# Performance work log

Measured on AMD Instinct MI355X. Metric: run time of the kernel, lower is better.

Reference implementation:

```python
import jax, jax.numpy as jnp
import numpy as np

N_NODES = 50000
N_EDGES = 800000
IN_FEATS = 128
OUT_FEATS = 128
FREQ_DIM = OUT_FEATS // 2 + 1
BN_EPS = 1e-5


def setup_inputs() -> dict:
    key = jax.random.key(0)
    ks = jax.random.split(key, 8)
    x = jax.random.normal(ks[0], (N_NODES, IN_FEATS), dtype=jnp.float32)
    edge_index = jax.random.randint(ks[1], (2, N_EDGES), 0, N_NODES, dtype=jnp.int64)
    # lin_fusion: Linear(2*in_feats, out_feats)
    W_fuse = jax.random.normal(ks[2], (OUT_FEATS, 2 * IN_FEATS), dtype=jnp.float32) * (1.0 / np.sqrt(2 * IN_FEATS))
    b_fuse = jnp.zeros((OUT_FEATS,), dtype=jnp.float32)
    # lin_in: Linear(in_feats, out_feats)
    W_in = jax.random.normal(ks[3], (OUT_FEATS, IN_FEATS), dtype=jnp.float32) * (1.0 / np.sqrt(IN_FEATS))
    b_in = jnp.zeros((OUT_FEATS,), dtype=jnp.float32)
    complex_weight = jax.random.normal(ks[4], (FREQ_DIM, 2), dtype=jnp.float32) * 0.02
    alpha = jnp.float32(0.5)
    gamma = jnp.ones((OUT_FEATS,), dtype=jnp.float32)
    beta = jnp.zeros((OUT_FEATS,), dtype=jnp.float32)
    return {"x": x, "edge_index": edge_index, "W_fuse": W_fuse, "b_fuse": b_fuse,
            "W_in": W_in, "b_in": b_in, "complex_weight": complex_weight,
            "alpha": alpha, "gamma": gamma, "beta": beta}


def reference(x, edge_index, W_fuse, b_fuse, W_in, b_in, complex_weight, alpha, gamma, beta):
    N = x.shape[0]
    src, dst = edge_index[0], edge_index[1]
    # --- spatial branch: scatter-mean aggregation of neighbor features ---
    msgs = x[src]  # [E, in] gather
    agg_sum = jax.ops.segment_sum(msgs, dst, num_segments=N)  # [N, in]
    cnt = jax.ops.segment_sum(jnp.ones((src.shape[0],), dtype=x.dtype), dst, num_segments=N)
    aggs = agg_sum / jnp.maximum(cnt, 1.0)[:, None]
    combined = jnp.concatenate([x, aggs], axis=1)  # [N, 2*in]
    x_spatial = combined @ W_fuse.T + b_fuse  # [N, out]
    # --- spectral branch: linear -> rfft * complex weight -> irfft ---
    h = x @ W_in.T + b_in  # [N, out]
    hf = jnp.fft.rfft(h, axis=-1)  # [N, out//2+1]
    w = complex_weight[:, 0] + 1j * complex_weight[:, 1]
    x_spectral = jnp.fft.irfft(hf * w, n=h.shape[-1], axis=-1).astype(x.dtype)
    # --- fuse + BatchNorm1d (training stats, biased var) + exact GELU ---
    out = x_spatial + alpha * x_spectral
    mean = jnp.mean(out, axis=0)
    var = jnp.mean(jnp.square(out - mean), axis=0)
    out = (out - mean) / jnp.sqrt(var + BN_EPS) * gamma + beta
    return jax.nn.gelu(out, approximate=False)
```

## Files before the change

kernel.cpp:

```cpp
#include <hip/hip_runtime.h>
#include <hip/hip_bf16.h>

#define NN 50000
#define NE 800000
#define FD 128
#define FREQ 65
#define CAP 64
#define BN_EPS 1e-5f

#define NB_PACK 3125
#define NB_CVT  6250
#define NB_WCB  128
#define NGRP 8
#define GRPN 6250
#define NCHUNK 256
#define CHUNKE 3125

typedef unsigned int u32;
typedef unsigned short u16;
typedef __attribute__((ext_vector_type(8))) short short8;
typedef __attribute__((ext_vector_type(4))) float float4v;
typedef __attribute__((ext_vector_type(2))) float floatx2;

__device__ __forceinline__ float bf2f(u16 v) {
    return __uint_as_float(((u32)v) << 16);
}
__device__ __forceinline__ u16 f2bf(float f) {
    u32 u = __float_as_uint(f);
    u32 lsb = (u >> 16) & 1u;
    return (u16)((u + 0x7fffu + lsb) >> 16);
}
__device__ __forceinline__ float ldf(const void* p, int i, int f32) {
    return f32 ? ((const float*)p)[i] : bf2f(((const u16*)p)[i]);
}
__device__ __forceinline__ int detect_f32(const void* gamma) {
    return ((const u32*)gamma)[0] == 0x3F800000u;
}
__device__ __forceinline__ int detect_idx64(const int* idx) {
    return (idx[1] | idx[3] | idx[5] | idx[7] |
            idx[9] | idx[11] | idx[13] | idx[15]) == 0;
}

__device__ __forceinline__ u32 pk4_e4m3(float a, float b, float c, float d) {
#if __has_builtin(__builtin_amdgcn_cvt_pk_fp8_f32)
    int r = __builtin_amdgcn_cvt_pk_fp8_f32(a, b, 0, false);
    r = __builtin_amdgcn_cvt_pk_fp8_f32(c, d, r, true);
    return (u32)r;
#else
    auto one = [](float f) -> u32 {
        u32 u = __float_as_uint(f);
        u32 s = (u >> 24) & 0x80u;
        float af = fabsf(f);
        if (af > 448.f) return s | 0x7Eu;
        if (af < 7.8125e-3f) return s;
        int e = (int)((u >> 23) & 255) - 127;
        u32 m = (u >> 20) & 7u;
        u32 rnd = (u >> 19) & 1u;
        u32 sticky = (u & 0x7FFFFu) ? 1u : 0u;
        m += (rnd & (sticky | (m & 1u)));
        u32 ee = (u32)(e + 7);
        if (m > 7u) { m = 0u; ee += 1u; }
        if (ee > 15u) return s | 0x7Eu;
        return s | (ee << 3) | m;
    };
    return one(a) | (one(b) << 8) | (one(c) << 16) | (one(d) << 24);
#endif
}
__device__ __forceinline__ void deq4_e4m3(u32 p, float& a, float& b, float& c, float& d) {
#if __has_builtin(__builtin_amdgcn_cvt_pk_f32_fp8)
    floatx2 lo = __builtin_amdgcn_cvt_pk_f32_fp8((int)p, false);
    floatx2 hi = __builtin_amdgcn_cvt_pk_f32_fp8((int)p, true);
    a = lo.x; b = lo.y; c = hi.x; d = hi.y;
#else
    auto one = [](u32 v) -> float {
        u32 s = (v & 0x80u) << 24;
        u32 e = (v >> 3) & 15u;
        u32 m = v & 7u;
        if (e == 0) {
            float f = (float)m * 0.001953125f;
            return s ? -f : f;
        }
        return __uint_as_float(s | ((e + 120u) << 23) | (m << 20));
    };
    a = one(p & 255u); b = one((p >> 8) & 255u);
    c = one((p >> 16) & 255u); d = one(p >> 24);
#endif
}

#define WS_WCB       0
#define WS_BIAS      65536
#define WS_ZSTART    66048
#define WS_BNSUM     66048
#define WS_BNSQ      66560
#define WS_DEG       67072
#define WS_ZEND      267072
#define WS_CSR16     267136
#define WS_EPACK     6667136
#define WS_X8        9867136
#define WS_OUT16     16267136

__global__ __launch_bounds__(256) void prep_kernel(const void* __restrict__ x,
                                                   const int* __restrict__ idx,
                                                   const void* __restrict__ Wf,
                                                   const void* __restrict__ bfu,
                                                   const void* __restrict__ Wi,
                                                   const void* __restrict__ bi,
                                                   const void* __restrict__ cw,
                                                   const void* __restrict__ alpha_p,
                                                   const void* __restrict__ gamma,
                                                   u32* __restrict__ epack,
                                                   u32* __restrict__ x8,
                                                   u16* __restrict__ WcB,
                                                   float* __restrict__ bias) {
    int b = blockIdx.x;
    int t = threadIdx.x;
    if (b < NB_PACK) {
        int e = b * 256 + t;
        int src, dst;
        if (detect_idx64(idx)) { src = idx[2 * e]; dst = idx[2 * NE + 2 * e]; }
        else                   { src = idx[e];     dst = idx[NE + e]; }
        epack[e] = ((u32)dst << 16) | (u32)src;
        return;
    }
    b -= NB_PACK;
    if (b < NB_CVT) {
        int gid = b * 256 + t;
        float a, bb, c, d;
        if (detect_f32(gamma)) {
            float4 v = ((const float4*)x)[gid];
            a = v.x; bb = v.y; c = v.z; d = v.w;
        } else {
            uint2 v = ((const uint2*)x)[gid];
            a = bf2f((u16)(v.x & 0xffffu)); bb = bf2f((u16)(v.x >> 16));
            c = bf2f((u16)(v.y & 0xffffu)); d = bf2f((u16)(v.y >> 16));
        }
        x8[gid] = pk4_e4m3(a, bb, c, d);
        return;
    }
    b -= NB_CVT;
    int f32 = detect_f32(gamma);
    int j = b;
    __shared__ float wr[FREQ], wi[FREQ];
    __shared__ float cl[128];
    __shared__ float part[256];
    if (t < FREQ) { wr[t] = ldf(cw, 2 * t, f32); wi[t] = ldf(cw, 2 * t + 1, f32); }
    __syncthreads();
    if (t < 128) {
        float s = wr[0] + ((t & 1) ? -wr[64] : wr[64]);
        for (int f = 1; f < 64; ++f) {
            int ph = (f * t) & 127;
            float th = (float)ph * (6.283185307179586f / 128.f);
            float sn, cs;
            sincosf(th, &sn, &cs);
            s += 2.f * (wr[f] * cs - wi[f] * sn);
        }
        cl[t] = s * (1.f / 128.f);
    }
    __syncthreads();
    int k = t & 127, mh = t >> 7;
    float acc = 0.f;
    int m0 = mh * 64;
#pragma unroll 8
    for (int mm = 0; mm < 64; ++mm) {
        int m = m0 + mm;
        acc = fmaf(ldf(Wi, m * 128 + k, f32), cl[(j - m) & 127], acc);
    }
    part[t] = acc;
    __syncthreads();
    if (t < 128) {
        float al = ldf(alpha_p, 0, f32);
        int ct = j >> 4;
        float v = ldf(Wf, j * 256 + k, f32) + al * (part[k] + part[k + 128]);
        int off = (((ct * 8 + (k >> 5)) * 64) + ((k >> 3) & 3) * 16 + (j & 15)) * 8 + (k & 7);
        WcB[off] = f2bf(v);
        int k2 = k + 128;
        float v2 = ldf(Wf, j * 256 + k2, f32);
        int off2 = (((ct * 8 + (k2 >> 5)) * 64) + ((k2 >> 3) & 3) * 16 + (j & 15)) * 8 + (k2 & 7);
        WcB[off2] = f2bf(v2);
        if (j == 0) {
            float bacc = 0.f;
            for (int m = 0; m < 128; ++m)
                bacc = fmaf(ldf(bi, m, f32), cl[(t - m) & 127], bacc);
            bias[t] = ldf(bfu, t, f32) + al * bacc;
        }
    }
}

__global__ __launch_bounds__(256) void bucket8_kernel(const u32* __restrict__ epack,
                                                      int* __restrict__ deg,
                                                      u16* __restrict__ csr) {
    int g = blockIdx.x & (NGRP - 1);
    int chunk = blockIdx.x >> 3;
    u32 lo = (u32)(g * GRPN) << 16;
    u32 hi = (u32)((g + 1) * GRPN) << 16;
    int base = chunk * CHUNKE;
    for (int i = threadIdx.x; i < CHUNKE; i += 256) {
        u32 p = epack[base + i];
        if (p >= lo && p < hi) {
            int dst = (int)(p >> 16);
            int pos = atomicAdd(deg + dst, 1);
            if (pos < CAP) csr[dst * CAP + pos] = (u16)(p & 0xffffu);
        }
    }
}

__global__ __launch_bounds__(256) void gemm_kernel(const void* __restrict__ x,
                                                   const u32* __restrict__ x8,
                                                   const u16* __restrict__ csr,
                                                   const int* __restrict__ deg,
                                                   const void* __restrict__ gamma,
                                                   const u16* __restrict__ WcB,
                                                   const float* __restrict__ bias,
                                                   u16* __restrict__ outp16,
                                                   float* __restrict__ bnsum,
                                                   float* __restrict__ bnsq) {
    __shared__ float lsum[FD], lsq[FD];
    __shared__ __align__(16) u16 lag[64 * FD];
    int t = threadIdx.x;
    if (t < FD) { lsum[t] = 0.f; lsq[t] = 0.f; }
    int f32 = detect_f32(gamma);
    int wave = t >> 6;
    int lane = t & 63;
    int n0 = blockIdx.x * 64;

    {
        int half = lane >> 5;
        int q = lane & 31;
        for (int nn = 0; nn < 8; ++nn) {
            int lrow = wave * 16 + half * 8 + nn;
            int node = n0 + lrow;
            int dcount = 0;
            u32 cv = 0;
            if (node < NN) {
                dcount = deg[node];
                cv = ((const u32*)csr)[(size_t)node * (CAP / 2) + q];
            }
            int cnt = min(dcount, CAP);
            float a0 = 0.f, a1 = 0.f, a2 = 0.f, a3 = 0.f;
            int jj = 0;
            while (jj < cnt) {
                int nb = cnt - jj;
                u32 p[8];
#pragma unroll
                for (int r = 0; r < 8; ++r) {
                    if (r < nb) {
                        u32 w = __shfl(cv, half * 32 + ((jj + r) >> 1));
                        u16 srcn = (u16)(w >> (((jj + r) & 1) * 16));
                        p[r] = x8[(size_t)srcn * 32 + q];
                    }
                }
#pragma unroll
                for (int r = 0; r < 8; ++r) {
                    if (r < nb) {
                        float b0, b1, b2, b3;
                        deq4_e4m3(p[r], b0, b1, b2, b3);
                        a0 += b0; a1 += b1; a2 += b2; a3 += b3;
                    }
                }
                jj += 8;
            }
            float rinv = 1.f / fmaxf((float)dcount, 1.f);
            uint2 w;
            w.x = (u32)f2bf(a0 * rinv) | ((u32)f2bf(a1 * rinv) << 16);
            w.y = (u32)f2bf(a2 * rinv) | ((u32)f2bf(a3 * rinv) << 16);
            ((uint2*)lag)[lrow * 32 + q] = w;
        }
    }
    __syncthreads();

    int quad = lane >> 4;
    int lm = lane & 15;
    int nrow = n0 + wave * 16 + lm;
    bool avalid = (nrow < NN);

    float4v acc[8];
#pragma unroll
    for (int ct = 0; ct < 8; ++ct) acc[ct] = (float4v){0.f, 0.f, 0.f, 0.f};

    const short8* bp = (const short8*)WcB;
#pragma unroll
    for (int ks = 0; ks < 8; ++ks) {
        short8 a = (short8)0;
        if (ks < 4) {
            if (avalid) {
                int k = ks * 32 + quad * 8;
                if (f32) {
                    const float4* p = (const float4*)x + (size_t)nrow * 32 + (k >> 2);
                    float4 v0 = p[0], v1 = p[1];
                    a[0] = (short)f2bf(v0.x); a[1] = (short)f2bf(v0.y);
                    a[2] = (short)f2bf(v0.z); a[3] = (short)f2bf(v0.w);
                    a[4] = (short)f2bf(v1.x); a[5] = (short)f2bf(v1.y);
                    a[6] = (short)f2bf(v1.z); a[7] = (short)f2bf(v1.w);
                } else {
                    a = ((const short8*)x)[(size_t)nrow * 16 + (k >> 3)];
                }
            }
        } else {
            int k = (ks - 4) * 32 + quad * 8;
            a = *(const short8*)&lag[(wave * 16 + lm) * FD + k];
        }
#pragma unroll
        for (int ct = 0; ct < 8; ++ct) {
            short8 b = bp[(ct * 8 + ks) * 64 + lane];
            acc[ct] = __builtin_amdgcn_mfma_f32_16x16x32_bf16(a, b, acc[ct], 0, 0, 0);
        }
    }

    int rbase = n0 + wave * 16 + quad * 4;
#pragma unroll
    for (int ct = 0; ct < 8; ++ct) {
        int col = ct * 16 + lm;
        float bj = bias[col];
        float s = 0.f, q = 0.f;
#pragma unroll
        for (int r = 0; r < 4; ++r) {
            int n = rbase + r;
            if (n < NN) {
                float v = acc[ct][r] + bj;
                outp16[(size_t)n * FD + col] = f2bf(v);
                s += v;
                q = fmaf(v, v, q);
            }
        }
        s += __shfl_xor(s, 16); s += __shfl_xor(s, 32);
        q += __shfl_xor(q, 16); q += __shfl_xor(q, 32);
        if (lane < 16) {
            atomicAdd(&lsum[col], s);
            atomicAdd(&lsq[col], q);
        }
    }
    __syncthreads();
    if (t < FD) {
        atomicAdd(bnsum + t, lsum[t]);
        atomicAdd(bnsq + t, lsq[t]);
    }
}

__global__ __launch_bounds__(256) void apply_kernel(const u32* __restrict__ outp16,
                                                    const float* __restrict__ bnsum,
                                                    const float* __restrict__ bnsq,
                                                    const void* __restrict__ gamma,
                                                    const void* __restrict__ beta,
                                                    void* __restrict__ out) {
    __shared__ float sc[FD], sh[FD];
    int t = threadIdx.x;
    int f32 = detect_f32(gamma);
    if (t < FD) {
        float mean = bnsum[t] * (1.f / NN);
        float var = bnsq[t] * (1.f / NN) - mean * mean;
        float s = ldf(gamma, t, f32) / sqrtf(var + BN_EPS);
        sc[t] = s;
        sh[t] = ldf(beta, t, f32) - mean * s;
    }
    __syncthreads();
    int gid = blockIdx.x * 256 + t;
    if (gid >= NN * (FD / 8)) return;
    uint4 pk = ((const uint4*)outp16)[gid];
    int f0 = (gid * 8) & 127;
    u32 w[4] = {pk.x, pk.y, pk.z, pk.w};
    float g[8];
#pragma unroll
    for (int q = 0; q < 4; ++q) {
        float v0 = bf2f((u16)(w[q] & 0xffffu));
        float v1 = bf2f((u16)(w[q] >> 16));
        float z0 = fmaf(v0, sc[f0 + 2 * q], sh[f0 + 2 * q]);
        float z1 = fmaf(v1, sc[f0 + 2 * q + 1], sh[f0 + 2 * q + 1]);
        g[2 * q]     = 0.5f * z0 * (1.f + erff(z0 * 0.70710678118654752f));
        g[2 * q + 1] = 0.5f * z1 * (1.f + erff(z1 * 0.70710678118654752f));
    }
    if (f32) {
        float4* o = (float4*)out + (size_t)gid * 2;
        o[0] = make_float4(g[0], g[1], g[2], g[3]);
        o[1] = make_float4(g[4], g[5], g[6], g[7]);
    } else {
        uint4 o;
        o.x = (u32)f2bf(g[0]) | ((u32)f2bf(g[1]) << 16);
        o.y = (u32)f2bf(g[2]) | ((u32)f2bf(g[3]) << 16);
        o.z = (u32)f2bf(g[4]) | ((u32)f2bf(g[5]) << 16);
        o.w = (u32)f2bf(g[6]) | ((u32)f2bf(g[7]) << 16);
        ((uint4*)out)[gid] = o;
    }
}

extern "C" void kernel_launch(void* const* d_in, const int* in_sizes, int n_in,
                              void* d_out, int out_size, void* d_ws, size_t ws_size,
                              hipStream_t stream) {
    const void* x     = d_in[0];
    const int* eidx   = (const int*)d_in[1];
    const void* Wf    = d_in[2];
    const void* bfu   = d_in[3];
    const void* Wi    = d_in[4];
    const void* bi    = d_in[5];
    const void* cw    = d_in[6];
    const void* alpha = d_in[7];
    const void* gamma = d_in[8];
    const void* beta  = d_in[9];

    char* ws = (char*)d_ws;
    u16*   WcB    = (u16*)(ws + WS_WCB);
    float* bias   = (float*)(ws + WS_BIAS);
    float* bnsum  = (float*)(ws + WS_BNSUM);
    float* bnsq   = (float*)(ws + WS_BNSQ);
    int*   deg    = (int*)(ws + WS_DEG);
    u16*   csr    = (u16*)(ws + WS_CSR16);
    u32*   epack  = (u32*)(ws + WS_EPACK);
    u32*   x8     = (u32*)(ws + WS_X8);
    u16*   outp16 = (u16*)(ws + WS_OUT16);

    hipMemsetAsync(ws + WS_ZSTART, 0, (size_t)WS_ZEND - WS_ZSTART, stream);

    prep_kernel<<<NB_PACK + NB_CVT + NB_WCB, 256, 0, stream>>>(
        x, eidx, Wf, bfu, Wi, bi, cw, alpha, gamma, epack, x8, WcB, bias);
    bucket8_kernel<<<NGRP * NCHUNK, 256, 0, stream>>>(epack, deg, csr);
    gemm_kernel<<<(NN + 63) / 64, 256, 0, stream>>>(x, x8, csr, deg, gamma, WcB,
                                                    bias, outp16, bnsum, bnsq);
    apply_kernel<<<(NN * (FD / 8) + 255) / 256, 256, 0, stream>>>((const u32*)outp16,
                                                                  bnsum, bnsq, gamma,
                                                                  beta, d_out);
}
```

Baseline: 251.8 us.

## Widen gather to 16-byte neighbor loads with 512-thread blocks

The neighbor aggregation in the fused GEMM kernel now has each 8-lane group load a full 16-byte slice of an fp8 row. Four neighbors are read in parallel per half-wave, and the partial sums are combined across lanes with shuffles. Blocks grow to 512 threads so that 4 nodes per half-wave cover 64 nodes. Only the first 256 threads run the MFMA GEMM stage. The aim is fewer, wider memory transactions and more gather parallelism, at the cost of extra shuffle reductions, higher register pressure, and idle waves during the GEMM stage.

New measurement: 248.3 us. No clear change (-1.4%).

```diff
diff --git a/kernel.cpp b/kernel.cpp
--- a/kernel.cpp
+++ b/kernel.cpp
@@ -204,129 +204,172 @@
     }
 }
 
-__global__ __launch_bounds__(256) void gemm_kernel(const void* __restrict__ x,
-                                                   const u32* __restrict__ x8,
-                                                   const u16* __restrict__ csr,
-                                                   const int* __restrict__ deg,
-                                                   const void* __restrict__ gamma,
-                                                   const u16* __restrict__ WcB,
-                                                   const float* __restrict__ bias,
-                                                   u16* __restrict__ outp16,
-                                                   float* __restrict__ bnsum,
-                                                   float* __restrict__ bnsq) {
+__device__ __forceinline__ uint4 ldrow(const uint4* __restrict__ x8v, u32 cv,
+                                       int h, int g, int rg, int cnt, int i0) {
+    uint4 P = make_uint4(0u, 0u, 0u, 0u);
+    if (i0 < cnt) {
+        int i  = i0 + rg;
+        int ii = min(i, cnt - 1);
+        u32 w  = __shfl(cv, h * 32 + (ii >> 1));
+        u32 srcn = (ii & 1) ? (w >> 16) : (w & 0xffffu);
+        P = x8v[(size_t)srcn * 8 + g];
+        if (i >= cnt) P = make_uint4(0u, 0u, 0u, 0u);
+    }
+    return P;
+}
+__device__ __forceinline__ void accrow(uint4 P, float* A) {
+    float b0, b1, b2, b3;
+    deq4_e4m3(P.x, b0, b1, b2, b3);
+    A[0] += b0; A[1] += b1; A[2] += b2; A[3] += b3;
+    deq4_e4m3(P.y, b0, b1, b2, b3);
+    A[4] += b0; A[5] += b1; A[6] += b2; A[7] += b3;
+    deq4_e4m3(P.z, b0, b1, b2, b3);
+    A[8] += b0; A[9] += b1; A[10] += b2; A[11] += b3;
+    deq4_e4m3(P.w, b0, b1, b2, b3);
+    A[12] += b0; A[13] += b1; A[14] += b2; A[15] += b3;
+}
+
+__global__ __launch_bounds__(512, 6) void gemm_kernel(const void* __restrict__ x,
+                                                      const u32* __restrict__ x8,
+                                                      const u16* __restrict__ csr,
+                                                      const int* __restrict__ deg,
+                                                      const void* __restrict__ gamma,
+                                                      const u16* __restrict__ WcB,
+                                                      const float* __restrict__ bias,
+                                                      u16* __restrict__ outp16,
+                                                      float* __restrict__ bnsum,
+                                                      float* __restrict__ bnsq) {
     __shared__ float lsum[FD], lsq[FD];
     __shared__ __align__(16) u16 lag[64 * FD];
     int t = threadIdx.x;
     if (t < FD) { lsum[t] = 0.f; lsq[t] = 0.f; }
     int f32 = detect_f32(gamma);
-    int wave = t >> 6;
     int lane = t & 63;
     int n0 = blockIdx.x * 64;
 
     {
-        int half = lane >> 5;
-        int q = lane & 31;
-        for (int nn = 0; nn < 8; ++nn) {
-            int lrow = wave * 16 + half * 8 + nn;
-            int node = n0 + lrow;
-            int dcount = 0;
-            u32 cv = 0;
-            if (node < NN) {
-                dcount = deg[node];
-                cv = ((const u32*)csr)[(size_t)node * (CAP / 2) + q];
-            }
-            int cnt = min(dcount, CAP);
-            float a0 = 0.f, a1 = 0.f, a2 = 0.f, a3 = 0.f;
-            int jj = 0;
-            while (jj < cnt) {
-                int nb = cnt - jj;
-                u32 p[8];
-#pragma unroll
-                for (int r = 0; r < 8; ++r) {
-                    if (r < nb) {
-                        u32 w = __shfl(cv, half * 32 + ((jj + r) >> 1));
-                        u16 srcn = (u16)(w >> (((jj + r) & 1) * 16));
-                        p[r] = x8[(size_t)srcn * 32 + q];
+        int hw = t >> 5;
+        int h  = (t >> 5) & 1;
+        int q  = lane & 31;
+        int g  = lane & 7;
+        int rg = (lane >> 3) & 3;
+        const uint4* x8v = (const uint4*)x8;
+        const u32* csrw = (const u32*)csr;
+
+        int dcs[4];
+        u32 cvs[4];
+#pragma unroll
+        for (int nn = 0; nn < 4; ++nn) {
+            int node = n0 + hw * 4 + nn;
+            dcs[nn] = (node < NN) ? deg[node] : 0;
+            cvs[nn] = (node < NN) ? csrw[(size_t)node * (CAP / 2) + q] : 0u;
+        }
+#pragma unroll
+        for (int nn = 0; nn < 4; ++nn) {
+            int lrow = hw * 4 + nn;
+            int dc = dcs[nn];
+            u32 cv = cvs[nn];
+            int cnt = min(dc, CAP);
+            float A[16];
+#pragma unroll
+            for (int f = 0; f < 16; ++f) A[f] = 0.f;
+            for (int jj = 0; jj < cnt; jj += 16) {
+                uint4 P0 = ldrow(x8v, cv, h, g, rg, cnt, jj);
+                uint4 P1 = ldrow(x8v, cv, h, g, rg, cnt, jj + 4);
+                uint4 P2 = ldrow(x8v, cv, h, g, rg, cnt, jj + 8);
+                uint4 P3 = ldrow(x8v, cv, h, g, rg, cnt, jj + 12);
+                accrow(P0, A); accrow(P1, A); accrow(P2, A); accrow(P3, A);
+            }
+#pragma unroll
+            for (int f = 0; f < 16; ++f) {
+                float v = A[f];
+                v += __shfl_xor(v, 8);
+                v += __shfl_xor(v, 16);
+                A[f] = v;
+            }
+            float rinv = 1.f / fmaxf((float)dc, 1.f);
+            if (rg < 2) {
+                float s0 = rg ? A[8]  : A[0];
+                float s1 = rg ? A[9]  : A[1];
+                float s2 = rg ? A[10] : A[2];
+                float s3 = rg ? A[11] : A[3];
+                float s4 = rg ? A[12] : A[4];
+                float s5 = rg ? A[13] : A[5];
+                float s6 = rg ? A[14] : A[6];
+                float s7 = rg ? A[15] : A[7];
+                uint4 W;
+                W.x = (u32)f2bf(s0 * rinv) | ((u32)f2bf(s1 * rinv) << 16);
+                W.y = (u32)f2bf(s2 * rinv) | ((u32)f2bf(s3 * rinv) << 16);
+                W.z = (u32)f2bf(s4 * rinv) | ((u32)f2bf(s5 * rinv) << 16);
+                W.w = (u32)f2bf(s6 * rinv) | ((u32)f2bf(s7 * rinv) << 16);
+                ((uint4*)lag)[lrow * 16 + g * 2 + rg] = W;
+            }
+        }
+    }
+    __syncthreads();
+
+    if (t < 256) {
+        int wave = t >> 6;
+        int quad = lane >> 4;
+        int lm = lane & 15;
+        int nrow = n0 + wave * 16 + lm;
+        bool avalid = (nrow < NN);
+
+        float4v acc[8];
+#pragma unroll
+        for (int ct = 0; ct < 8; ++ct) acc[ct] = (float4v){0.f, 0.f, 0.f, 0.f};
+
+        const short8* bp = (const short8*)WcB;
+#pragma unroll
+        for (int ks = 0; ks < 8; ++ks) {
+            short8 a = (short8)0;
+            if (ks < 4) {
+                if (avalid) {
+                    int k = ks * 32 + quad * 8;
+                    if (f32) {
+                        const float4* p = (const float4*)x + (size_t)nrow * 32 + (k >> 2);
+                        float4 v0 = p[0], v1 = p[1];
+                        a[0] = (short)f2bf(v0.x); a[1] = (short)f2bf(v0.y);
+                        a[2] = (short)f2bf(v0.z); a[3] = (short)f2bf(v0.w);
+                        a[4] = (short)f2bf(v1.x); a[5] = (short)f2bf(v1.y);
+                        a[6] = (short)f2bf(v1.z); a[7] = (short)f2bf(v1.w);
+                    } else {
+                        a = ((const short8*)x)[(size_t)nrow * 16 + (k >> 3)];
                     }
                 }
-#pragma unroll
-                for (int r = 0; r < 8; ++r) {
-                    if (r < nb) {
-                        float b0, b1, b2, b3;
-                        deq4_e4m3(p[r], b0, b1, b2, b3);
-                        a0 += b0; a1 += b1; a2 += b2; a3 += b3;
-                    }
+            } else {
+                int k = (ks - 4) * 32 + quad * 8;
+                a = *(const short8*)&lag[(wave * 16 + lm) * FD + k];
+            }
+#pragma unroll
+            for (int ct = 0; ct < 8; ++ct) {
+                short8 b = bp[(ct * 8 + ks) * 64 + lane];
+                acc[ct] = __builtin_amdgcn_mfma_f32_16x16x32_bf16(a, b, acc[ct], 0, 0, 0);
+            }
+        }
+
+        int rbase = n0 + wave * 16 + quad * 4;
+#pragma unroll
+        for (int ct = 0; ct < 8; ++ct) {
+            int col = ct * 16 + lm;
+            float bj = bias[col];
+            float s = 0.f, q = 0.f;
+#pragma unroll
+            for (int r = 0; r < 4; ++r) {
+                int n = rbase + r;
+                if (n < NN) {
+                    float v = acc[ct][r] + bj;
+                    outp16[(size_t)n * FD + col] = f2bf(v);
+                    s += v;
+                    q = fmaf(v, v, q);
                 }
-                jj += 8;
-            }
-            float rinv = 1.f / fmaxf((float)dcount, 1.f);
-            uint2 w;
-            w.x = (u32)f2bf(a0 * rinv) | ((u32)f2bf(a1 * rinv) << 16);
-            w.y = (u32)f2bf(a2 * rinv) | ((u32)f2bf(a3 * rinv) << 16);
-            ((uint2*)lag)[lrow * 32 + q] = w;
-        }
-    }
-    __syncthreads();
-
-    int quad = lane >> 4;
-    int lm = lane & 15;
-    int nrow = n0 + wave * 16 + lm;
-    bool avalid = (nrow < NN);
-
-    float4v acc[8];
-#pragma unroll
-    for (int ct = 0; ct < 8; ++ct) acc[ct] = (float4v){0.f, 0.f, 0.f, 0.f};
-
-    const short8* bp = (const short8*)WcB;
-#pragma unroll
-    for (int ks = 0; ks < 8; ++ks) {
-        short8 a = (short8)0;
-        if (ks < 4) {
-            if (avalid) {
-                int k = ks * 32 + quad * 8;
-                if (f32) {
-                    const float4* p = (const float4*)x + (size_t)nrow * 32 + (k >> 2);
-                    float4 v0 = p[0], v1 = p[1];
-                    a[0] = (short)f2bf(v0.x); a[1] = (short)f2bf(v0.y);
-                    a[2] = (short)f2bf(v0.z); a[3] = (short)f2bf(v0.w);
-                    a[4] = (short)f2bf(v1.x); a[5] = (short)f2bf(v1.y);
-                    a[6] = (short)f2bf(v1.z); a[7] = (short)f2bf(v1.w);
-                } else {
-                    a = ((const short8*)x)[(size_t)nrow * 16 + (k >> 3)];
-                }
-            }
-        } else {
-            int k = (ks - 4) * 32 + quad * 8;
-            a = *(const short8*)&lag[(wave * 16 + lm) * FD + k];
-        }
-#pragma unroll
-        for (int ct = 0; ct < 8; ++ct) {
-            short8 b = bp[(ct * 8 + ks) * 64 + lane];
-            acc[ct] = __builtin_amdgcn_mfma_f32_16x16x32_bf16(a, b, acc[ct], 0, 0, 0);
-        }
-    }
-
-    int rbase = n0 + wave * 16 + quad * 4;
-#pragma unroll
-    for (int ct = 0; ct < 8; ++ct) {
-        int col = ct * 16 + lm;
-        float bj = bias[col];
-        float s = 0.f, q = 0.f;
-#pragma unroll
-        for (int r = 0; r < 4; ++r) {
-            int n = rbase + r;
-            if (n < NN) {
-                float v = acc[ct][r] + bj;
-                outp16[(size_t)n * FD + col] = f2bf(v);
-                s += v;
-                q = fmaf(v, v, q);
-            }
-        }
-        s += __shfl_xor(s, 16); s += __shfl_xor(s, 32);
-        q += __shfl_xor(q, 16); q += __shfl_xor(q, 32);
-        if (lane < 16) {
-            atomicAdd(&lsum[col], s);
-            atomicAdd(&lsq[col], q);
+            }
+            s += __shfl_xor(s, 16); s += __shfl_xor(s, 32);
+            q += __shfl_xor(q, 16); q += __shfl_xor(q, 32);
+            if (lane < 16) {
+                atomicAdd(&lsum[col], s);
+                atomicAdd(&lsq[col], q);
+            }
         }
     }
     __syncthreads();
@@ -412,7 +455,7 @@
     prep_kernel<<<NB_PACK + NB_CVT + NB_WCB, 256, 0, stream>>>(
         x, eidx, Wf, bfu, Wi, bi, cw, alpha, gamma, epack, x8, WcB, bias);
     bucket8_kernel<<<NGRP * NCHUNK, 256, 0, stream>>>(epack, deg, csr);
-    gemm_kernel<<<(NN + 63) / 64, 256, 0, stream>>>(x, x8, csr, deg, gamma, WcB,
+    gemm_kernel<<<(NN + 63) / 64, 512, 0, stream>>>(x, x8, csr, deg, gamma, WcB,
                                                     bias, outp16, bnsum, bnsq);
     apply_kernel<<<(NN * (FD / 8) + 255) / 256, 256, 0, stream>>>((const u32*)outp16,
                                                                   bnsum, bnsq, gamma,
```
